# Kernel tuning notes

Measured on AMD Instinct MI355X. Metric: run time of the kernel, lower is better.

The kernel has to match this reference:

```python
import jax, jax.numpy as jnp
import numpy as np

H = W = 1536
DT = 0.02
FAST_DT, SLOW_DT = 1.0, 0.2
EPS_FAST, EPS_SLOW = 0.06, 0.02
F2S, S2F = 0.04, 0.02


def setup_inputs() -> dict:
    key = jax.random.key(0)
    k1, k2, k3 = jax.random.split(key, 3)
    phi = jax.random.normal(k1, (1, 10, H, W), jnp.float32)
    sensory_map = jax.random.normal(k2, (1, 1, H, W), jnp.float32)
    gamma = jnp.array([0.2, 0.15, 0.1, 0.18, 0.12, 0.13, 0.14, 0.16, 0.11, 0.1], jnp.float32)
    alpha = jnp.array([0.3, 0.25, 0.22, 0.18, 0.2, 0.15, 0.19, 0.24, 0.17, 0.16], jnp.float32)
    mix_w = jax.random.normal(k3, (10, 10), jnp.float32) * 0.1  # 1x1 conv weight, no bias
    return {"phi": phi, "sensory_map": sensory_map, "gamma": gamma, "alpha": alpha, "mix_w": mix_w}


def _lap(x):
    # periodic 5-point Laplacian via rolls on the last two (spatial) dims
    return (jnp.roll(x, 1, -2) + jnp.roll(x, -1, -2)
            + jnp.roll(x, 1, -1) + jnp.roll(x, -1, -1) - 4.0 * x)


def _step(phi, sensory_map, gamma, alpha, mix_w):
    lap = _lap(phi)
    bilap = _lap(lap)
    g, a, p = gamma, alpha, phi
    ch = [
        -g[0] * lap[:, 0] - a[0] * p[:, 0] ** 3 + 0.12 * bilap[:, 0],
        -g[1] * lap[:, 1] + 0.15 * jnp.sin(p[:, 1]) + 0.08 * p[:, 1] ** 3,
        -g[2] * lap[:, 2] + 0.2 * p[:, 2] * (1.0 - p[:, 2] ** 2),
        -g[3] * lap[:, 3] - 0.03 * p[:, 3] ** 5 + 0.08 * bilap[:, 3],
        -g[4] * lap[:, 4] + 0.12 * p[:, 4] * jnp.log(jnp.abs(p[:, 4]) + 1e-6) + 0.02 * bilap[:, 4],
        -g[5] * lap[:, 5] + 0.08 * p[:, 5] ** 3 - 0.02 * p[:, 5] ** 5,
        -g[6] * lap[:, 6] + 0.06 * p[:, 6] ** 4 - 0.04 * p[:, 6],
        -g[7] * lap[:, 7] + 0.08 * jnp.sinh(jnp.clip(p[:, 7], -2.0, 2.0)),
        -g[8] * lap[:, 8] + 0.05 * p[:, 8] ** 2 - 0.08 * p[:, 8],
        -g[9] * lap[:, 9] + 0.02 * p[:, 9] ** 6 - 0.04 * p[:, 9] ** 3 + 0.01 * bilap[:, 9],
    ]
    dphi = jnp.stack(ch, axis=1)                                 # [1,10,H,W]
    coupling = jnp.einsum('oc,bchw->bohw', mix_w, phi)            # 1x1 conv, no bias
    fast_mean = phi[:, :5].mean(axis=1, keepdims=True)            # [1,1,H,W]
    slow_mean = phi[:, 5:].mean(axis=1, keepdims=True)
    sd = sensory_map[:, 0]                                        # [1,H,W]
    dphi_f = dphi[:, :5] + EPS_FAST * coupling[:, :5] + S2F * slow_mean
    dphi_s = dphi[:, 5:] + EPS_SLOW * coupling[:, 5:] + F2S * fast_mean
    dphi_f = dphi_f.at[:, 0].add(0.2 * sd).at[:, 4].add(0.08 * jnp.abs(sd))
    dphi_s = dphi_s.at[:, 4].add(0.05 * sd)                       # global channel 9
    phi_next = jnp.concatenate([phi[:, :5] + DT * FAST_DT * dphi_f,
                                phi[:, 5:] + DT * SLOW_DT * dphi_s], axis=1)
    return jnp.clip(phi_next, -4.0, 4.0)


def reference(phi, sensory_map, gamma, alpha, mix_w):
    phi_next = _step(phi, sensory_map, gamma, alpha, mix_w)
    phi1_mean = phi_next[:, 0].mean(axis=(1, 2))
    phi5_mean = phi_next[:, 4].mean(axis=(1, 2))
    field_means = phi_next.mean(axis=(2, 3))
    return phi_next, phi1_mean, phi5_mean, field_means
```

## Files before the change

### kernel.cpp

```cpp
#include <hip/hip_runtime.h>
#include <math.h>

#define HH 1536
#define WW 1536
#define HWSZ (HH*WW)
#define NT 256
#define NBLK ((HH*WW/4)/NT)
#define BPX (NBLK/8)

__device__ __forceinline__ float4 LD4(const float* __restrict__ p, int row, int idx) {
    return reinterpret_cast<const float4*>(p + row)[idx];
}

__global__ __launch_bounds__(NT, 4) void step_kernel(
    const float* __restrict__ phi,
    const float* __restrict__ sensory,
    const float* __restrict__ gamma,
    const float* __restrict__ alpha,
    const float* __restrict__ mixw,
    float* __restrict__ out,
    float* __restrict__ sums)
{
    __shared__ float s_mix[10][12];
    __shared__ float s_red[4][10];

    const int tid = threadIdx.x;
    if (tid < 100) s_mix[tid / 10][tid % 10] = mixw[tid];

    const int b  = blockIdx.x;
    const int nb = (b & 7) * BPX + (b >> 3);

    const int lane = tid & 63;
    const int wave = tid >> 6;
    const int gw   = nb * 4 + wave;
    const int y    = gw / 6;
    const int wseg = gw - y * 6;
    const int col  = wseg * 64 + lane;
    const int x0   = col * 4;

    const int ym1 = (y == 0)      ? HH - 1     : y - 1;
    const int yp1 = (y == HH - 1) ? 0          : y + 1;
    const int ym2 = (y < 2)       ? y + HH - 2 : y - 2;
    const int yp2 = (y >= HH - 2) ? y - HH + 2 : y + 2;

    const int r0  = y   * WW;
    const int rm1 = ym1 * WW;
    const int rp1 = yp1 * WW;
    const int rm2 = ym2 * WW;
    const int rp2 = yp2 * WW;

    const int xl1 = (x0 == 0)      ? WW - 1 : x0 - 1;
    const int xl2 = (x0 == 0)      ? WW - 2 : x0 - 2;
    const int xr1 = (x0 + 4 == WW) ? 0      : x0 + 4;
    const int xr2 = (x0 + 4 == WW) ? 1      : x0 + 5;

    const float g0 = gamma[0], g1 = gamma[1], g2 = gamma[2], g3 = gamma[3], g4 = gamma[4];
    const float g5 = gamma[5], g6 = gamma[6], g7 = gamma[7], g8 = gamma[8], g9 = gamma[9];
    const float a0 = alpha[0];

    float pv[10][4];
    float dv[10][4];

    #pragma unroll
    for (int c = 0; c < 10; ++c) {
        const float* pc = phi + (size_t)c * HWSZ;
        const float4 cm = LD4(pc, r0,  col);
        const float4 nn = LD4(pc, rm1, col);
        const float4 ss = LD4(pc, rp1, col);

        float wl1 = __shfl_up  (cm.w, 1, 64);
        float wr1 = __shfl_down(cm.x, 1, 64);

        const bool BI = (c == 0 || c == 3 || c == 4 || c == 9);
        float4 t2n = {0,0,0,0}, t2s = {0,0,0,0};
        float wl2 = 0.f, wr2 = 0.f, nwl = 0.f, ner = 0.f, swl = 0.f, ser = 0.f;
        if (BI) {
            t2n = LD4(pc, rm2, col);
            t2s = LD4(pc, rp2, col);
            wl2 = __shfl_up  (cm.z, 1, 64);
            wr2 = __shfl_down(cm.y, 1, 64);
            nwl = __shfl_up  (nn.w, 1, 64);
            ner = __shfl_down(nn.x, 1, 64);
            swl = __shfl_up  (ss.w, 1, 64);
            ser = __shfl_down(ss.x, 1, 64);
        }
        if (lane == 0) {
            wl1 = pc[r0 + xl1];
            if (BI) { wl2 = pc[r0 + xl2]; nwl = pc[rm1 + xl1]; swl = pc[rp1 + xl1]; }
        }
        if (lane == 63) {
            wr1 = pc[r0 + xr1];
            if (BI) { wr2 = pc[r0 + xr2]; ner = pc[rm1 + xr1]; ser = pc[rp1 + xr1]; }
        }

        float lap[4];
        lap[0] = nn.x + ss.x + wl1  + cm.y - 4.0f * cm.x;
        lap[1] = nn.y + ss.y + cm.x + cm.z - 4.0f * cm.y;
        lap[2] = nn.z + ss.z + cm.y + cm.w - 4.0f * cm.z;
        lap[3] = nn.w + ss.w + cm.z + wr1  - 4.0f * cm.w;

        float bl[4] = {0.f, 0.f, 0.f, 0.f};
        if (BI) {
            bl[0] = 20.0f*cm.x - 8.0f*(nn.x + ss.x + wl1  + cm.y)
                  + 2.0f*(nwl  + nn.y + swl  + ss.y) + (t2n.x + t2s.x + wl2  + cm.z);
            bl[1] = 20.0f*cm.y - 8.0f*(nn.y + ss.y + cm.x + cm.z)
                  + 2.0f*(nn.x + nn.z + ss.x + ss.z) + (t2n.y + t2s.y + wl1  + cm.w);
            bl[2] = 20.0f*cm.z - 8.0f*(nn.z + ss.z + cm.y + cm.w)
                  + 2.0f*(nn.y + nn.w + ss.y + ss.w) + (t2n.z + t2s.z + cm.x + wr1);
            bl[3] = 20.0f*cm.w - 8.0f*(nn.w + ss.w + cm.z + wr1)
                  + 2.0f*(nn.z + ner  + ss.z + ser ) + (t2n.w + t2s.w + cm.y + wr2);
        }

        pv[c][0] = cm.x; pv[c][1] = cm.y; pv[c][2] = cm.z; pv[c][3] = cm.w;

        #pragma unroll
        for (int k = 0; k < 4; ++k) {
            const float pp = pv[c][k];
            const float lv = lap[k];
            const float bv = bl[k];
            float dd;
            switch (c) {
            case 0: dd = -g0*lv - a0*pp*pp*pp + 0.12f*bv; break;
            case 1: dd = -g1*lv + 0.15f*__sinf(pp) + 0.08f*pp*pp*pp; break;
            case 2: dd = -g2*lv + 0.2f*pp*(1.0f - pp*pp); break;
            case 3: { const float p2 = pp*pp;
                      dd = -g3*lv - 0.03f*p2*p2*pp + 0.08f*bv; } break;
            case 4: dd = -g4*lv + 0.12f*pp*__logf(fabsf(pp) + 1e-6f) + 0.02f*bv; break;
            case 5: { const float p2 = pp*pp;
                      dd = -g5*lv + 0.08f*p2*pp - 0.02f*p2*p2*pp; } break;
            case 6: { const float p2 = pp*pp;
                      dd = -g6*lv + 0.06f*p2*p2 - 0.04f*pp; } break;
            case 7: { const float pc7 = fminf(fmaxf(pp, -2.0f), 2.0f);
                      const float ex  = __expf(pc7);
                      const float exm = __expf(-pc7);
                      dd = -g7*lv + 0.04f*(ex - exm); } break;
            case 8: dd = -g8*lv + 0.05f*pp*pp - 0.08f*pp; break;
            default: { const float p3 = pp*pp*pp;
                       dd = -g9*lv + 0.02f*p3*p3 - 0.04f*p3 + 0.01f*bv; } break;
            }
            dv[c][k] = dd;
        }
    }

    float fmv[4], smv[4], sdk[4];
    {
        const float4 sd4 = LD4(sensory, r0, col);
        sdk[0] = sd4.x; sdk[1] = sd4.y; sdk[2] = sd4.z; sdk[3] = sd4.w;
        #pragma unroll
        for (int k = 0; k < 4; ++k) {
            fmv[k] = (pv[0][k] + pv[1][k] + pv[2][k] + pv[3][k] + pv[4][k]) * 0.2f;
            smv[k] = (pv[5][k] + pv[6][k] + pv[7][k] + pv[8][k] + pv[9][k]) * 0.2f;
        }
    }

    __syncthreads();

    #pragma unroll
    for (int o = 0; o < 10; ++o) {
        const float4 m0 = *reinterpret_cast<const float4*>(&s_mix[o][0]);
        const float4 m1 = *reinterpret_cast<const float4*>(&s_mix[o][4]);
        const float2 m2 = *reinterpret_cast<const float2*>(&s_mix[o][8]);
        float pn[4];
        #pragma unroll
        for (int k = 0; k < 4; ++k) {
            float cp;
            cp = m0.x * pv[0][k];
            cp = fmaf(m0.y, pv[1][k], cp);
            cp = fmaf(m0.z, pv[2][k], cp);
            cp = fmaf(m0.w, pv[3][k], cp);
            cp = fmaf(m1.x, pv[4][k], cp);
            cp = fmaf(m1.y, pv[5][k], cp);
            cp = fmaf(m1.z, pv[6][k], cp);
            cp = fmaf(m1.w, pv[7][k], cp);
            cp = fmaf(m2.x, pv[8][k], cp);
            cp = fmaf(m2.y, pv[9][k], cp);
            float dd = dv[o][k];
            if (o < 5) {
                dd += 0.06f * cp + 0.02f * smv[k];
                if (o == 0) dd += 0.2f  * sdk[k];
                if (o == 4) dd += 0.08f * fabsf(sdk[k]);
                pn[k] = pv[o][k] + 0.02f * dd;
            } else {
                dd += 0.02f * cp + 0.04f * fmv[k];
                if (o == 9) dd += 0.05f * sdk[k];
                pn[k] = pv[o][k] + 0.004f * dd;
            }
            pn[k] = fminf(fmaxf(pn[k], -4.0f), 4.0f);
        }
        float4 o4; o4.x = pn[0]; o4.y = pn[1]; o4.z = pn[2]; o4.w = pn[3];
        reinterpret_cast<float4*>(out + (size_t)o * HWSZ + r0)[col] = o4;

        float s = pn[0] + pn[1] + pn[2] + pn[3];
        #pragma unroll
        for (int off = 32; off > 0; off >>= 1) s += __shfl_down(s, off, 64);
        if (lane == 0) s_red[wave][o] = s;
    }

    __syncthreads();
    if (tid < 10) {
        float v = s_red[0][tid] + s_red[1][tid] + s_red[2][tid] + s_red[3][tid];
        atomicAdd(&sums[tid], v);
    }
}

__global__ void finalize_kernel(const float* __restrict__ sums,
                                float* __restrict__ out)
{
    const int t = threadIdx.x;
    const float inv = 1.0f / (float)HWSZ;
    const size_t base = (size_t)10 * HWSZ;
    if (t == 0) out[base]     = sums[0] * inv;
    if (t == 1) out[base + 1] = sums[4] * inv;
    if (t >= 2 && t < 12) out[base + 2 + (t - 2)] = sums[t - 2] * inv;
}

extern "C" void kernel_launch(void* const* d_in, const int* in_sizes, int n_in,
                              void* d_out, int out_size, void* d_ws, size_t ws_size,
                              hipStream_t stream) {
    const float* phi     = (const float*)d_in[0];
    const float* sensory = (const float*)d_in[1];
    const float* gamma   = (const float*)d_in[2];
    const float* alpha   = (const float*)d_in[3];
    const float* mixw    = (const float*)d_in[4];
    float* out = (float*)d_out;
    float* sums = (float*)d_ws;

    hipMemsetAsync(sums, 0, 10 * sizeof(float), stream);

    step_kernel<<<dim3(NBLK), NT, 0, stream>>>(phi, sensory, gamma, alpha, mixw, out, sums);
    finalize_kernel<<<1, 64, 0, stream>>>(sums, out);
}
```

Baseline: 297.8 us.

## Map one row per 384-thread block and fuse finalize via last-block counter

Each block now covers one full image row with 384 threads instead of 256-thread blocks spread over partial rows, with row order interleaved across blocks. The separate finalize launch is removed: a counter in workspace marks the last block, which reads the accumulated sums and writes the means. This saves one kernel launch and simplifies index math. In exchange it drops the occupancy hint in launch_bounds and adds a threadfence plus atomic counter per block.

After: 267.5 us. 10.2% less time.

```diff
diff --git a/kernel.cpp b/kernel.cpp
--- a/kernel.cpp
+++ b/kernel.cpp
@@ -4,15 +4,15 @@
 #define HH 1536
 #define WW 1536
 #define HWSZ (HH*WW)
-#define NT 256
-#define NBLK ((HH*WW/4)/NT)
-#define BPX (NBLK/8)
-
-__device__ __forceinline__ float4 LD4(const float* __restrict__ p, int row, int idx) {
-    return reinterpret_cast<const float4*>(p + row)[idx];
+#define NT 384
+#define NBLK HH
+
+
+__device__ __forceinline__ float4 LD4(const float* __restrict__ p, int row, int t) {
+    return reinterpret_cast<const float4*>(p + row)[t];
 }
 
-__global__ __launch_bounds__(NT, 4) void step_kernel(
+__global__ __launch_bounds__(NT) void step_kernel(
     const float* __restrict__ phi,
     const float* __restrict__ sensory,
     const float* __restrict__ gamma,
@@ -22,21 +22,17 @@
     float* __restrict__ sums)
 {
     __shared__ float s_mix[10][12];
-    __shared__ float s_red[4][10];
+    __shared__ float s_red[6][10];
 
     const int tid = threadIdx.x;
     if (tid < 100) s_mix[tid / 10][tid % 10] = mixw[tid];
 
-    const int b  = blockIdx.x;
-    const int nb = (b & 7) * BPX + (b >> 3);
+    const int blk = blockIdx.x;
+    const int y = (blk & 7) * 192 + (blk >> 3);
 
     const int lane = tid & 63;
     const int wave = tid >> 6;
-    const int gw   = nb * 4 + wave;
-    const int y    = gw / 6;
-    const int wseg = gw - y * 6;
-    const int col  = wseg * 64 + lane;
-    const int x0   = col * 4;
+    const int x0 = tid * 4;
 
     const int ym1 = (y == 0)      ? HH - 1     : y - 1;
     const int yp1 = (y == HH - 1) ? 0          : y + 1;
@@ -64,9 +60,9 @@
     #pragma unroll
     for (int c = 0; c < 10; ++c) {
         const float* pc = phi + (size_t)c * HWSZ;
-        const float4 cm = LD4(pc, r0,  col);
-        const float4 nn = LD4(pc, rm1, col);
-        const float4 ss = LD4(pc, rp1, col);
+        const float4 cm = LD4(pc, r0,  tid);
+        const float4 nn = LD4(pc, rm1, tid);
+        const float4 ss = LD4(pc, rp1, tid);
 
         float wl1 = __shfl_up  (cm.w, 1, 64);
         float wr1 = __shfl_down(cm.x, 1, 64);
@@ -75,8 +71,8 @@
         float4 t2n = {0,0,0,0}, t2s = {0,0,0,0};
         float wl2 = 0.f, wr2 = 0.f, nwl = 0.f, ner = 0.f, swl = 0.f, ser = 0.f;
         if (BI) {
-            t2n = LD4(pc, rm2, col);
-            t2s = LD4(pc, rp2, col);
+            t2n = LD4(pc, rm2, tid);
+            t2s = LD4(pc, rp2, tid);
             wl2 = __shfl_up  (cm.z, 1, 64);
             wr2 = __shfl_down(cm.y, 1, 64);
             nwl = __shfl_up  (nn.w, 1, 64);
@@ -144,7 +140,7 @@
 
     float fmv[4], smv[4], sdk[4];
     {
-        const float4 sd4 = LD4(sensory, r0, col);
+        const float4 sd4 = LD4(sensory, r0, tid);
         sdk[0] = sd4.x; sdk[1] = sd4.y; sdk[2] = sd4.z; sdk[3] = sd4.w;
         #pragma unroll
         for (int k = 0; k < 4; ++k) {
@@ -188,7 +184,7 @@
             pn[k] = fminf(fmaxf(pn[k], -4.0f), 4.0f);
         }
         float4 o4; o4.x = pn[0]; o4.y = pn[1]; o4.z = pn[2]; o4.w = pn[3];
-        reinterpret_cast<float4*>(out + (size_t)o * HWSZ + r0)[col] = o4;
+        reinterpret_cast<float4*>(out + (size_t)o * HWSZ + r0)[tid] = o4;
 
         float s = pn[0] + pn[1] + pn[2] + pn[3];
         #pragma unroll
@@ -198,20 +194,29 @@
 
     __syncthreads();
     if (tid < 10) {
-        float v = s_red[0][tid] + s_red[1][tid] + s_red[2][tid] + s_red[3][tid];
+        float v = 0.0f;
+        #pragma unroll
+        for (int w = 0; w < 6; ++w) v += s_red[w][tid];
         atomicAdd(&sums[tid], v);
     }
-}
-
-__global__ void finalize_kernel(const float* __restrict__ sums,
-                                float* __restrict__ out)
-{
-    const int t = threadIdx.x;
-    const float inv = 1.0f / (float)HWSZ;
-    const size_t base = (size_t)10 * HWSZ;
-    if (t == 0) out[base]     = sums[0] * inv;
-    if (t == 1) out[base + 1] = sums[4] * inv;
-    if (t >= 2 && t < 12) out[base + 2 + (t - 2)] = sums[t - 2] * inv;
+
+    __syncthreads();
+    if (tid == 0) {
+        __threadfence();
+        unsigned int* cnt = reinterpret_cast<unsigned int*>(sums + 10);
+        const unsigned int old = atomicAdd(cnt, 1u);
+        if (old == (unsigned int)(NBLK - 1)) {
+            const float inv = 1.0f / (float)HWSZ;
+            const size_t base = (size_t)10 * HWSZ;
+            float sv[10];
+            #pragma unroll
+            for (int i = 0; i < 10; ++i) sv[i] = atomicAdd(&sums[i], 0.0f);
+            out[base]     = sv[0] * inv;
+            out[base + 1] = sv[4] * inv;
+            #pragma unroll
+            for (int i = 0; i < 10; ++i) out[base + 2 + i] = sv[i] * inv;
+        }
+    }
 }
 
 extern "C" void kernel_launch(void* const* d_in, const int* in_sizes, int n_in,
@@ -225,8 +230,7 @@
     float* out = (float*)d_out;
     float* sums = (float*)d_ws;
 
-    hipMemsetAsync(sums, 0, 10 * sizeof(float), stream);
+    hipMemsetAsync(sums, 0, 11 * sizeof(float), stream);
 
     step_kernel<<<dim3(NBLK), NT, 0, stream>>>(phi, sensory, gamma, alpha, mixw, out, sums);
-    finalize_kernel<<<1, 64, 0, stream>>>(sums, out);
 }
```
